# Kernel tuning notes

Measured on AMD Instinct MI355X. Metric: run time of the kernel, lower is better.

The kernel has to match this reference:

```python
import jax, jax.numpy as jnp
import numpy as np

N, E, D, L = 100000, 500000, 128, 5
NUM_ATOM_FEATS, ATOM_VOCAB = 9, 120
NUM_BOND_FEATS, BOND_VOCAB = 3, 8
BN_EPS = 1e-5


def setup_inputs() -> dict:
    key = jax.random.key(0)
    ks = jax.random.split(key, 16)
    inp = {
        "x": jax.random.randint(ks[0], (N, NUM_ATOM_FEATS), 0, ATOM_VOCAB),
        "edge_index": jax.random.randint(ks[1], (2, E), 0, N),
        "edge_attr": jax.random.randint(ks[2], (E, NUM_BOND_FEATS), 0, BOND_VOCAB),
        "edge_weight": jax.random.uniform(ks[3], (E,), dtype=jnp.float32),
        # parameters
        "atom_emb": jax.random.normal(ks[4], (NUM_ATOM_FEATS, ATOM_VOCAB, D), dtype=jnp.float32) * 0.02,
        "bond_emb": jax.random.normal(ks[5], (L, NUM_BOND_FEATS, BOND_VOCAB, D), dtype=jnp.float32) * 0.02,
        "eps": jnp.zeros((L,), dtype=jnp.float32),
        "W1": jax.random.normal(ks[6], (L, D, 2 * D), dtype=jnp.float32) / np.sqrt(D),
        "b1": jnp.zeros((L, 2 * D), dtype=jnp.float32),
        "g1": jnp.ones((L, 2 * D), dtype=jnp.float32),
        "bt1": jnp.zeros((L, 2 * D), dtype=jnp.float32),
        "W2": jax.random.normal(ks[7], (L, 2 * D, D), dtype=jnp.float32) / np.sqrt(2 * D),
        "b2": jnp.zeros((L, D), dtype=jnp.float32),
        "g_out": jnp.ones((L, D), dtype=jnp.float32),
        "bt_out": jnp.zeros((L, D), dtype=jnp.float32),
    }
    return inp


def _batchnorm(h, g, b):
    # training-mode BN over node axis, biased variance (matches torch BN normalization)
    mu = jnp.mean(h, axis=0)
    var = jnp.mean((h - mu) ** 2, axis=0)
    return g * (h - mu) * jax.lax.rsqrt(var + BN_EPS) + b


def reference(x, edge_index, edge_attr, edge_weight,
              atom_emb, bond_emb, eps, W1, b1, g1, bt1, W2, b2, g_out, bt_out):
    # AtomEncoder: sum per-column embedding lookups -> [N, D]
    h = atom_emb[jnp.arange(NUM_ATOM_FEATS)[None, :], x].sum(axis=1)
    src, dst = edge_index[0], edge_index[1]
    ew = edge_weight[:, None]
    for l in range(L):
        # BondEncoder for layer l -> [E, D]
        e = bond_emb[l][jnp.arange(NUM_BOND_FEATS)[None, :], edge_attr].sum(axis=1)
        # message: relu(x_j + edge_emb) * edge_weight ; aggregate: scatter-add at dst
        m = jax.nn.relu(h[src] + e) * ew
        agg = jax.ops.segment_sum(m, dst, num_segments=N)
        z = (1.0 + eps[l]) * h + agg
        # GIN MLP: Linear -> BN -> ReLU -> Linear
        z = jax.nn.relu(_batchnorm(z @ W1[l] + b1[l], g1[l], bt1[l])) @ W2[l] + b2[l]
        # outer BatchNorm; dropout is identity in eval mode
        h_new = _batchnorm(z, g_out[l], bt_out[l])
        h = h_new if l == L - 1 else jax.nn.relu(h_new)
    return h
```

## Files before the change

### kernel.cpp

```cpp
#include <hip/hip_runtime.h>
#include <hip/hip_bf16.h>
#include <hip/hip_fp16.h>

#define NN 100000
#define EE 500000
#define NP 100096

typedef _Float16 f16;
typedef __attribute__((ext_vector_type(8))) _Float16 f16x8;
typedef __attribute__((ext_vector_type(4))) _Float16 f16x4;
typedef __attribute__((ext_vector_type(4))) float f32x4;

static __device__ __forceinline__ f16x8 relu8(f16x8 a) {
#if __has_builtin(__builtin_elementwise_max)
  f16x8 z = {0, 0, 0, 0, 0, 0, 0, 0};
  return __builtin_elementwise_max(a, z);
#else
  f16x8 r;
#pragma unroll
  for (int i = 0; i < 8; ++i) r[i] = (a[i] > (f16)0) ? a[i] : (f16)0;
  return r;
#endif
}

__global__ __launch_bounds__(256) void init_kernel(const float* __restrict__ W1,
                                                   const float* __restrict__ W2,
                                                   f16* __restrict__ w1f,
                                                   f16* __restrict__ w2f,
                                                   int* __restrict__ deg,
                                                   float* __restrict__ slices) {
  int gid = blockIdx.x * 256 + threadIdx.x;
  if (gid < 163840) {
    int l = gid / 32768; int rem = gid % 32768;
    int k = rem / 256;   int n = rem % 256;
    int ctg = n >> 4, m = n & 15;
    int c = k >> 5, q = (k >> 3) & 3, e = k & 7;
    int lane = q * 16 + m;
    w1f[l * 32768 + ((ctg * 4 + c) * 64 + lane) * 8 + e] = (f16)W1[gid];
  } else if (gid < 327680) {
    int g = gid - 163840;
    int l = g / 32768; int rem = g % 32768;
    int k = rem / 128; int n = rem % 128;
    int ctg = n >> 4, m = n & 15;
    int c = k >> 5, q = (k >> 3) & 3, e = k & 7;
    int lane = q * 16 + m;
    w2f[l * 32768 + ((ctg * 8 + c) * 64 + lane) * 8 + e] = (f16)W2[g];
  } else if (gid < 427680) {
    int i = gid - 327680;
    if (i < NN) deg[i] = 0;
  } else if (gid < 439968) {
    slices[gid - 427680] = 0.f;
  }
}

__global__ __launch_bounds__(256) void bondtab_kernel(const float* __restrict__ bemb,
                                                      f16* __restrict__ tab) {
  int gid = blockIdx.x * 256 + threadIdx.x;
  int l = gid >> 16;
  int rem = gid & 65535;
  int combo = rem >> 7, d = rem & 127;
  int a0 = combo & 7, a1 = (combo >> 3) & 7, a2 = combo >> 6;
  const float* bl = bemb + l * 3072;
  float v = bl[a0 * 128 + d] + bl[1024 + a1 * 128 + d] + bl[2048 + a2 * 128 + d];
  tab[gid] = (f16)v;
}

__global__ __launch_bounds__(256) void hist_kernel(const int* __restrict__ ei, int* __restrict__ deg) {
  int e = blockIdx.x * 256 + threadIdx.x;
  if (e < EE) atomicAdd(&deg[ei[EE + e]], 1);
}

__global__ __launch_bounds__(256) void scan1_kernel(const int* __restrict__ deg,
                                                    int* __restrict__ offs,
                                                    int* __restrict__ bsum) {
  __shared__ int sh[256];
  int b = blockIdx.x, t = threadIdx.x;
  int base = b * 1024 + t * 4;
  int v[4];
  int s = 0;
#pragma unroll
  for (int i = 0; i < 4; ++i) { v[i] = (base + i < NN) ? deg[base + i] : 0; s += v[i]; }
  sh[t] = s;
  __syncthreads();
  for (int off = 1; off < 256; off <<= 1) {
    int x = (t >= off) ? sh[t - off] : 0;
    __syncthreads();
    sh[t] += x;
    __syncthreads();
  }
  int excl = sh[t] - s;
  if (t == 255) bsum[b] = sh[255];
  int run = excl;
#pragma unroll
  for (int i = 0; i < 4; ++i) {
    if (base + i < NN) offs[base + i] = run;
    run += v[i];
  }
}

__global__ void scan2_kernel(int* __restrict__ bsum, int nb) {
  if (threadIdx.x == 0 && blockIdx.x == 0) {
    int run = 0;
    for (int i = 0; i < nb; ++i) { int v = bsum[i]; bsum[i] = run; run += v; }
  }
}

__global__ __launch_bounds__(256) void scan3_kernel(int* __restrict__ offs,
                                                    const int* __restrict__ bsum,
                                                    int* __restrict__ cursor) {
  int i = blockIdx.x * 256 + threadIdx.x;
  if (i < NN) {
    int v = offs[i] + bsum[i >> 10];
    offs[i] = v;
    cursor[i] = v;
  } else if (i == NN) {
    offs[NN] = EE;
  }
}

__global__ __launch_bounds__(256) void scatter_kernel(const int* __restrict__ ei,
                                                      const int* __restrict__ ea,
                                                      const float* __restrict__ ew,
                                                      int* __restrict__ cursor,
                                                      int2* __restrict__ pkw) {
  int e = blockIdx.x * 256 + threadIdx.x;
  if (e >= EE) return;
  int dst = ei[EE + e];
  int pos = atomicAdd(&cursor[dst], 1);
  int src = ei[e];
  int a0 = ea[e * 3 + 0], a1 = ea[e * 3 + 1], a2 = ea[e * 3 + 2];
  pkw[pos] = make_int2(src | (a0 << 17) | (a1 << 20) | (a2 << 23), __float_as_int(ew[e]));
}

__global__ __launch_bounds__(256) void atom_kernel(const int* __restrict__ x,
                                                   const float* __restrict__ aemb,
                                                   f16* __restrict__ hf) {
  int gid = blockIdx.x * 256 + threadIdx.x;
  int n = gid >> 5, qq = gid & 31;
  if (n >= NN) return;
  float4 s = {0.f, 0.f, 0.f, 0.f};
#pragma unroll
  for (int f = 0; f < 9; ++f) {
    int xi = x[n * 9 + f];
    float4 v = *(const float4*)(aemb + (f * 120 + xi) * 128 + qq * 4);
    s.x += v.x; s.y += v.y; s.z += v.z; s.w += v.w;
  }
  f16x4 o;
  o[0] = (f16)s.x; o[1] = (f16)s.y; o[2] = (f16)s.z; o[3] = (f16)s.w;
  *(f16x4*)(hf + (long)n * 128 + qq * 4) = o;
}

__global__ __launch_bounds__(256) void edge_agg_kernel(const int* __restrict__ offs,
                                                       const int2* __restrict__ pkw,
                                                       const f16* __restrict__ tab,
                                                       const float* __restrict__ eps,
                                                       const f16* __restrict__ hf,
                                                       f16* __restrict__ zb) {
  int gid = blockIdx.x * 256 + threadIdx.x;
  int n = gid >> 4, d0 = (gid & 15) * 8;
  if (n >= NN) {
    f16x8 z = {0, 0, 0, 0, 0, 0, 0, 0};
    *(f16x8*)(zb + (long)n * 128 + d0) = z;
    return;
  }
  int s0 = offs[n], s1 = offs[n + 1];
  float e1 = 1.f + eps[0];
  f16x8 hn = *(const f16x8*)(hf + (long)n * 128 + d0);
  float acc[8];
#pragma unroll
  for (int i = 0; i < 8; ++i) acc[i] = e1 * (float)hn[i];

  float wA, wB; f16x8 hA, bA, hB, bB;
  if (s0 < s1) {
    int2 pw = pkw[s0]; wA = __int_as_float(pw.y);
    hA = *(const f16x8*)(hf + (long)(pw.x & 131071) * 128 + d0);
    bA = *(const f16x8*)(tab + ((pw.x >> 17) & 511) * 128 + d0);
  }
  if (s0 + 1 < s1) {
    int2 pw = pkw[s0 + 1]; wB = __int_as_float(pw.y);
    hB = *(const f16x8*)(hf + (long)(pw.x & 131071) * 128 + d0);
    bB = *(const f16x8*)(tab + ((pw.x >> 17) & 511) * 128 + d0);
  }
  int e = s0;
  for (; e + 1 < s1; e += 2) {
    {
      f16x8 sm = relu8(hA + bA);
#pragma unroll
      for (int i = 0; i < 8; ++i) acc[i] += (float)sm[i] * wA;
      if (e + 2 < s1) {
        int2 pw = pkw[e + 2]; wA = __int_as_float(pw.y);
        hA = *(const f16x8*)(hf + (long)(pw.x & 131071) * 128 + d0);
        bA = *(const f16x8*)(tab + ((pw.x >> 17) & 511) * 128 + d0);
      }
    }
    {
      f16x8 sm = relu8(hB + bB);
#pragma unroll
      for (int i = 0; i < 8; ++i) acc[i] += (float)sm[i] * wB;
      if (e + 3 < s1) {
        int2 pw = pkw[e + 3]; wB = __int_as_float(pw.y);
        hB = *(const f16x8*)(hf + (long)(pw.x & 131071) * 128 + d0);
        bB = *(const f16x8*)(tab + ((pw.x >> 17) & 511) * 128 + d0);
      }
    }
  }
  if (e < s1) {
    f16x8 sm = relu8(hA + bA);
#pragma unroll
    for (int i = 0; i < 8; ++i) acc[i] += (float)sm[i] * wA;
  }
  f16x8 o;
#pragma unroll
  for (int i = 0; i < 8; ++i) o[i] = (f16)acc[i];
  *(f16x8*)(zb + (long)n * 128 + d0) = o;
}

__global__ __launch_bounds__(256) void edge_agg_bn_kernel(const int* __restrict__ offs,
                                                          const int2* __restrict__ pkw,
                                                          const f16* __restrict__ tab,
                                                          const float* __restrict__ eps, int l,
                                                          const f16* __restrict__ t2,
                                                          const float* __restrict__ sum2s,
                                                          const float* __restrict__ sq2s,
                                                          const float* __restrict__ g2,
                                                          const float* __restrict__ bt2,
                                                          float* __restrict__ s1z,
                                                          f16* __restrict__ zb) {
  __shared__ float sc2[128], sh2[128];
  const int tid = threadIdx.x;
  if (tid < 128) {
    float s = 0.f, s2 = 0.f;
#pragma unroll
    for (int k = 0; k < 16; ++k) { s += sum2s[k * 128 + tid]; s2 += sq2s[k * 128 + tid]; }
    float mu = s * (1.f / NN);
    float var = fmaxf(s2 * (1.f / NN) - mu * mu, 0.f);
    float is = rsqrtf(var + 1e-5f);
    float sc = g2[tid] * is;
    sc2[tid] = sc;
    sh2[tid] = bt2[tid] - mu * sc;
  }
  if (blockIdx.x == 0) {
#pragma unroll
    for (int j = 0; j < 8; ++j)
      *(float4*)(s1z + (j * 256 + tid) * 4) = float4{0.f, 0.f, 0.f, 0.f};
  }
  __syncthreads();
  int gid = blockIdx.x * 256 + tid;
  int n = gid >> 4, d0 = (gid & 15) * 8;
  if (n >= NN) {
    f16x8 z = {0, 0, 0, 0, 0, 0, 0, 0};
    *(f16x8*)(zb + (long)n * 128 + d0) = z;
    return;
  }
  float4 svA = *(const float4*)(sc2 + d0), svB = *(const float4*)(sc2 + d0 + 4);
  float4 shA = *(const float4*)(sh2 + d0), shB = *(const float4*)(sh2 + d0 + 4);
  float sv[8] = {svA.x, svA.y, svA.z, svA.w, svB.x, svB.y, svB.z, svB.w};
  float hv[8] = {shA.x, shA.y, shA.z, shA.w, shB.x, shB.y, shB.z, shB.w};
  f16x8 sv8, hv8;
#pragma unroll
  for (int i = 0; i < 8; ++i) { sv8[i] = (f16)sv[i]; hv8[i] = (f16)hv[i]; }

  int s0 = offs[n], s1 = offs[n + 1];
  float e1 = 1.f + eps[l];
  f16x8 hn = *(const f16x8*)(t2 + (long)n * 128 + d0);
  float acc[8];
#pragma unroll
  for (int i = 0; i < 8; ++i)
    acc[i] = e1 * fmaxf((float)hn[i] * sv[i] + hv[i], 0.f);

  float wA, wB; f16x8 hA, bA, hB, bB;
  if (s0 < s1) {
    int2 pw = pkw[s0]; wA = __int_as_float(pw.y);
    hA = *(const f16x8*)(t2 + (long)(pw.x & 131071) * 128 + d0);
    bA = *(const f16x8*)(tab + ((pw.x >> 17) & 511) * 128 + d0);
  }
  if (s0 + 1 < s1) {
    int2 pw = pkw[s0 + 1]; wB = __int_as_float(pw.y);
    hB = *(const f16x8*)(t2 + (long)(pw.x & 131071) * 128 + d0);
    bB = *(const f16x8*)(tab + ((pw.x >> 17) & 511) * 128 + d0);
  }
  int e = s0;
  for (; e + 1 < s1; e += 2) {
    {
      f16x8 y = relu8(hA * sv8 + hv8);
      f16x8 sm = relu8(y + bA);
#pragma unroll
      for (int i = 0; i < 8; ++i) acc[i] += (float)sm[i] * wA;
      if (e + 2 < s1) {
        int2 pw = pkw[e + 2]; wA = __int_as_float(pw.y);
        hA = *(const f16x8*)(t2 + (long)(pw.x & 131071) * 128 + d0);
        bA = *(const f16x8*)(tab + ((pw.x >> 17) & 511) * 128 + d0);
      }
    }
    {
      f16x8 y = relu8(hB * sv8 + hv8);
      f16x8 sm = relu8(y + bB);
#pragma unroll
      for (int i = 0; i < 8; ++i) acc[i] += (float)sm[i] * wB;
      if (e + 3 < s1) {
        int2 pw = pkw[e + 3]; wB = __int_as_float(pw.y);
        hB = *(const f16x8*)(t2 + (long)(pw.x & 131071) * 128 + d0);
        bB = *(const f16x8*)(tab + ((pw.x >> 17) & 511) * 128 + d0);
      }
    }
  }
  if (e < s1) {
    f16x8 y = relu8(hA * sv8 + hv8);
    f16x8 sm = relu8(y + bA);
#pragma unroll
    for (int i = 0; i < 8; ++i) acc[i] += (float)sm[i] * wA;
  }
  f16x8 o;
#pragma unroll
  for (int i = 0; i < 8; ++i) o[i] = (f16)acc[i];
  *(f16x8*)(zb + (long)n * 128 + d0) = o;
}

__global__ __launch_bounds__(256) void gemm1_kernel(const f16* __restrict__ zb,
                                                    const f16* __restrict__ w1f,
                                                    f16* __restrict__ t1f,
                                                    float* __restrict__ sum1s,
                                                    float* __restrict__ sq1s,
                                                    float* __restrict__ s2z) {
  __shared__ __align__(16) char ldsraw[17408];
  const int tid = threadIdx.x;
  const int lane = tid & 63, w = tid >> 6;
  const int wr = w >> 1, wc = w & 1;
  const int m = lane & 15, q = lane >> 4;
  const int rbase = blockIdx.x * 64;
  const int slice = blockIdx.x & 15;

  if (blockIdx.x == 0) {
#pragma unroll
    for (int j = 0; j < 4; ++j)
      *(float4*)(s2z + (j * 256 + tid) * 4) = float4{0.f, 0.f, 0.f, 0.f};
  }

  {
    f16x8 st[4];
    const int tofs = tid * 16;
#pragma unroll
    for (int j = 0; j < 4; ++j)
      st[j] = *(const f16x8*)(zb + (long)rbase * 128 + (tofs + j * 4096) / 2);
#pragma unroll
    for (int j = 0; j < 4; ++j) {
      int ofs = tofs + j * 4096;
      int row = ofs >> 8, colb = ofs & 255;
      *(f16x8*)(ldsraw + row * 256 + (colb ^ ((row & 7) << 4))) = st[j];
    }
  }
  __syncthreads();

  f16x8 A[2][4];
#pragma unroll
  for (int rt = 0; rt < 2; ++rt) {
    int row = wr * 32 + rt * 16 + m;
    int rs = row * 256, sw = (row & 7) << 4;
#pragma unroll
    for (int c = 0; c < 4; ++c) {
      int colb = c * 64 + q * 16;
      A[rt][c] = *(const f16x8*)(ldsraw + rs + (colb ^ sw));
    }
  }
  __syncthreads();

  f16 (*sh)[136] = (f16(*)[136])ldsraw;
  const int colc = tid & 15, r0 = tid >> 4;

#pragma unroll
  for (int h = 0; h < 2; ++h) {
    f16x8 B[4][4];
#pragma unroll
    for (int ct = 0; ct < 4; ++ct)
#pragma unroll
      for (int c = 0; c < 4; ++c)
        B[ct][c] = *(const f16x8*)(w1f + (((h * 8 + wc * 4 + ct) * 4 + c) * 64 + lane) * 8);

    f32x4 acc[2][4];
    const f32x4 zf = {0.f, 0.f, 0.f, 0.f};
#pragma unroll
    for (int a = 0; a < 2; ++a)
#pragma unroll
      for (int b = 0; b < 4; ++b) acc[a][b] = zf;
#pragma unroll
    for (int c = 0; c < 4; ++c)
#pragma unroll
      for (int rt = 0; rt < 2; ++rt)
#pragma unroll
        for (int ct = 0; ct < 4; ++ct)
          acc[rt][ct] = __builtin_amdgcn_mfma_f32_16x16x32_f16(A[rt][c], B[ct][c], acc[rt][ct], 0, 0, 0);

#pragma unroll
    for (int ct = 0; ct < 4; ++ct) {
      int lc = wc * 64 + ct * 16 + m;
      int gc = h * 128 + lc;
      float s = 0.f, s2 = 0.f;
#pragma unroll
      for (int rt = 0; rt < 2; ++rt) {
        int lr = wr * 32 + rt * 16 + q * 4;
#pragma unroll
        for (int i = 0; i < 4; ++i) {
          float v = acc[rt][ct][i];
          s += v; s2 += v * v;
          sh[lr + i][lc] = (f16)v;
        }
      }
      s  += __shfl_xor(s, 16);  s  += __shfl_xor(s, 32);
      s2 += __shfl_xor(s2, 16); s2 += __shfl_xor(s2, 32);
      if (q == 0) {
        unsafeAtomicAdd(&sum1s[slice * 256 + gc], s);
        unsafeAtomicAdd(&sq1s[slice * 256 + gc], s2);
      }
    }
    __syncthreads();
#pragma unroll
    for (int j = 0; j < 4; ++j) {
      int r = j * 16 + r0;
      f16x8 v = *(const f16x8*)(&sh[r][colc * 8]);
      *(f16x8*)(t1f + (long)(rbase + r) * 256 + h * 128 + colc * 8) = v;
    }
    __syncthreads();
  }
}

__global__ __launch_bounds__(256) void gemm2_kernel(const f16* __restrict__ a1,
                                                    const f16* __restrict__ w2f,
                                                    const float* __restrict__ sum1s,
                                                    const float* __restrict__ sq1s,
                                                    const float* __restrict__ g1,
                                                    const float* __restrict__ bt1,
                                                    f16* __restrict__ t2out,
                                                    float* __restrict__ sum2s,
                                                    float* __restrict__ sq2s) {
  __shared__ __align__(16) char ldsraw[34816];
  float* sc1 = (float*)(ldsraw + 32768);
  float* sh1 = (float*)(ldsraw + 33792);
  const int tid = threadIdx.x;
  const int lane = tid & 63, w = tid >> 6;
  const int wr = w >> 1, wc = w & 1;
  const int m = lane & 15, q = lane >> 4;
  const int rbase = blockIdx.x * 64;
  const int slice = blockIdx.x & 15;

  f16x8 st[8];
  const int tofs = tid * 16;
#pragma unroll
  for (int j = 0; j < 8; ++j)
    st[j] = *(const f16x8*)(a1 + (long)rbase * 256 + (tofs + j * 4096) / 2);

  {
    float s = 0.f, s2 = 0.f;
#pragma unroll
    for (int k = 0; k < 16; ++k) { s += sum1s[k * 256 + tid]; s2 += sq1s[k * 256 + tid]; }
    float mu = s * (1.f / NN);
    float var = fmaxf(s2 * (1.f / NN) - mu * mu, 0.f);
    float is = rsqrtf(var + 1e-5f);
    float sc = g1[tid] * is;
    sc1[tid] = sc;
    sh1[tid] = bt1[tid] - mu * sc;
  }
  __syncthreads();

  {
    const int k0 = (tid & 31) * 8;
    float4 sa = *(const float4*)(sc1 + k0);
    float4 sb = *(const float4*)(sc1 + k0 + 4);
    float4 ha = *(const float4*)(sh1 + k0);
    float4 hb = *(const float4*)(sh1 + k0 + 4);
#pragma unroll
    for (int j = 0; j < 8; ++j) {
      int ofs = tofs + j * 4096;
      int row = ofs >> 9, colb = ofs & 511;
      f16x8 u = st[j], o;
      o[0] = (f16)fmaxf((float)u[0] * sa.x + ha.x, 0.f);
      o[1] = (f16)fmaxf((float)u[1] * sa.y + ha.y, 0.f);
      o[2] = (f16)fmaxf((float)u[2] * sa.z + ha.z, 0.f);
      o[3] = (f16)fmaxf((float)u[3] * sa.w + ha.w, 0.f);
      o[4] = (f16)fmaxf((float)u[4] * sb.x + hb.x, 0.f);
      o[5] = (f16)fmaxf((float)u[5] * sb.y + hb.y, 0.f);
      o[6] = (f16)fmaxf((float)u[6] * sb.z + hb.z, 0.f);
      o[7] = (f16)fmaxf((float)u[7] * sb.w + hb.w, 0.f);
      *(f16x8*)(ldsraw + row * 512 + (colb ^ ((row & 7) << 4))) = o;
    }
  }
  __syncthreads();

  f32x4 acc[2][4];
  const f32x4 zf = {0.f, 0.f, 0.f, 0.f};
#pragma unroll
  for (int a = 0; a < 2; ++a)
#pragma unroll
    for (int b = 0; b < 4; ++b) acc[a][b] = zf;

#pragma unroll
  for (int hh = 0; hh < 2; ++hh) {
    f16x8 A[2][4], B[4][4];
#pragma unroll
    for (int rt = 0; rt < 2; ++rt) {
      int row = wr * 32 + rt * 16 + m;
      int rs = row * 512, sw = (row & 7) << 4;
#pragma unroll
      for (int c = 0; c < 4; ++c) {
        int colb = (hh * 4 + c) * 64 + q * 16;
        A[rt][c] = *(const f16x8*)(ldsraw + rs + (colb ^ sw));
      }
    }
#pragma unroll
    for (int ct = 0; ct < 4; ++ct)
#pragma unroll
      for (int c = 0; c < 4; ++c)
        B[ct][c] = *(const f16x8*)(w2f + (((wc * 4 + ct) * 8 + hh * 4 + c) * 64 + lane) * 8);
#pragma unroll
    for (int c = 0; c < 4; ++c)
#pragma unroll
      for (int rt = 0; rt < 2; ++rt)
#pragma unroll
        for (int ct = 0; ct < 4; ++ct)
          acc[rt][ct] = __builtin_amdgcn_mfma_f32_16x16x32_f16(A[rt][c], B[ct][c], acc[rt][ct], 0, 0, 0);
  }

  __syncthreads();
  f16 (*sh)[136] = (f16(*)[136])ldsraw;

#pragma unroll
  for (int ct = 0; ct < 4; ++ct) {
    int gc = wc * 64 + ct * 16 + m;
    float s = 0.f, s2 = 0.f;
#pragma unroll
    for (int rt = 0; rt < 2; ++rt) {
      int grow = rbase + wr * 32 + rt * 16 + q * 4;
      int lr = wr * 32 + rt * 16 + q * 4;
#pragma unroll
      for (int i = 0; i < 4; ++i) {
        float v = acc[rt][ct][i];
        float vv = (grow + i < NN) ? v : 0.f;
        s += vv; s2 += vv * vv;
        sh[lr + i][gc] = (f16)v;
      }
    }
    s  += __shfl_xor(s, 16);  s  += __shfl_xor(s, 32);
    s2 += __shfl_xor(s2, 16); s2 += __shfl_xor(s2, 32);
    if (q == 0) {
      unsafeAtomicAdd(&sum2s[slice * 128 + gc], s);
      unsafeAtomicAdd(&sq2s[slice * 128 + gc], s2);
    }
  }
  __syncthreads();
  const int colc = tid & 15, r0 = tid >> 4;
#pragma unroll
  for (int j = 0; j < 4; ++j) {
    int r = j * 16 + r0;
    f16x8 v = *(const f16x8*)(&sh[r][colc * 8]);
    *(f16x8*)(t2out + (long)(rbase + r) * 128 + colc * 8) = v;
  }
}

__global__ __launch_bounds__(256) void apply_kernel(const f16* __restrict__ t2,
                                                    const float* __restrict__ sum2s,
                                                    const float* __restrict__ sq2s,
                                                    const float* __restrict__ g2,
                                                    const float* __restrict__ bt2,
                                                    float* __restrict__ outp) {
  __shared__ float sc2[128], sh2[128];
  const int tid = threadIdx.x;
  if (tid < 128) {
    float s = 0.f, s2 = 0.f;
#pragma unroll
    for (int k = 0; k < 16; ++k) { s += sum2s[k * 128 + tid]; s2 += sq2s[k * 128 + tid]; }
    float mu = s * (1.f / NN);
    float var = fmaxf(s2 * (1.f / NN) - mu * mu, 0.f);
    float is = rsqrtf(var + 1e-5f);
    float sc = g2[tid] * is;
    sc2[tid] = sc;
    sh2[tid] = bt2[tid] - mu * sc;
  }
  __syncthreads();
  const int rbase = blockIdx.x * 64;
#pragma unroll
  for (int k = 0; k < 4; ++k) {
    int ci = tid + k * 256;
    int r = ci >> 4, c8 = ci & 15;
    int row = rbase + r;
    if (row >= NN) continue;
    f16x8 u = *(const f16x8*)(t2 + (long)row * 128 + c8 * 8);
    float4 sa = *(const float4*)(sc2 + c8 * 8);
    float4 sb = *(const float4*)(sc2 + c8 * 8 + 4);
    float4 ha = *(const float4*)(sh2 + c8 * 8);
    float4 hb = *(const float4*)(sh2 + c8 * 8 + 4);
    float4 o0 = {(float)u[0] * sa.x + ha.x, (float)u[1] * sa.y + ha.y,
                 (float)u[2] * sa.z + ha.z, (float)u[3] * sa.w + ha.w};
    float4 o1 = {(float)u[4] * sb.x + hb.x, (float)u[5] * sb.y + hb.y,
                 (float)u[6] * sb.z + hb.z, (float)u[7] * sb.w + hb.w};
    *(float4*)(outp + (long)row * 128 + c8 * 8) = o0;
    *(float4*)(outp + (long)row * 128 + c8 * 8 + 4) = o1;
  }
}

extern "C" void kernel_launch(void* const* d_in, const int* in_sizes, int n_in,
                              void* d_out, int out_size, void* d_ws, size_t ws_size,
                              hipStream_t stream) {
  (void)in_sizes; (void)n_in; (void)out_size; (void)ws_size;
  const int*   x      = (const int*)d_in[0];
  const int*   ei     = (const int*)d_in[1];
  const int*   ea     = (const int*)d_in[2];
  const float* ew     = (const float*)d_in[3];
  const float* aemb   = (const float*)d_in[4];
  const float* bemb   = (const float*)d_in[5];
  const float* eps    = (const float*)d_in[6];
  const float* W1     = (const float*)d_in[7];
  const float* g1     = (const float*)d_in[9];
  const float* bt1    = (const float*)d_in[10];
  const float* W2     = (const float*)d_in[11];
  const float* g_out  = (const float*)d_in[13];
  const float* bt_out = (const float*)d_in[14];

  float* outp = (float*)d_out;

  char* ws = (char*)d_ws;
  f16*   hf    = (f16*)(ws);
  f16*   zb    = (f16*)(ws + 25624576);
  f16*   t1f   = (f16*)(ws + 51249152);
  f16*   w1f   = (f16*)(ws + 102498304);
  f16*   w2f   = (f16*)(ws + 102825984);
  float* slices= (float*)(ws + 103153664);
  int*   offs  = (int*)(ws + 103202816);
  int*   bsum  = (int*)(ws + 103602848);
  int*   deg   = (int*)(ws + 103603360);
  int*   cursor= (int*)(ws + 104003360);
  f16*   bsumtab = (f16*)(ws + 103603360);
  int2*  pkw   = (int2*)(ws + 104403360);

  float* sum1s = slices;
  float* sq1s  = slices + 4096;
  float* sum2s = slices + 8192;
  float* sq2s  = slices + 10240;

  init_kernel<<<1719, 256, 0, stream>>>(W1, W2, w1f, w2f, deg, slices);
  hist_kernel<<<1954, 256, 0, stream>>>(ei, deg);
  scan1_kernel<<<98, 256, 0, stream>>>(deg, offs, bsum);
  scan2_kernel<<<1, 64, 0, stream>>>(bsum, 98);
  scan3_kernel<<<392, 256, 0, stream>>>(offs, bsum, cursor);
  scatter_kernel<<<1954, 256, 0, stream>>>(ei, ea, ew, cursor, pkw);
  bondtab_kernel<<<1280, 256, 0, stream>>>(bemb, bsumtab);
  atom_kernel<<<12500, 256, 0, stream>>>(x, aemb, hf);

  for (int l = 0; l < 5; ++l) {
    if (l == 0) {
      edge_agg_kernel<<<6256, 256, 0, stream>>>(offs, pkw, bsumtab, eps, hf, zb);
    } else {
      edge_agg_bn_kernel<<<6256, 256, 0, stream>>>(offs, pkw, bsumtab + l * 65536, eps, l,
                                                   hf, sum2s, sq2s,
                                                   g_out + (l - 1) * 128, bt_out + (l - 1) * 128,
                                                   sum1s, zb);
    }
    gemm1_kernel<<<1564, 256, 0, stream>>>(zb, w1f + l * 32768, t1f, sum1s, sq1s, sum2s);
    gemm2_kernel<<<1564, 256, 0, stream>>>(t1f, w2f + l * 32768, sum1s, sq1s,
                                           g1 + l * 256, bt1 + l * 256, hf, sum2s, sq2s);
    if (l == 4)
      apply_kernel<<<1564, 256, 0, stream>>>(hf, sum2s, sq2s, g_out + 512, bt_out + 512, outp);
  }
}
```

Before: 597.1 us.

## Sort nodes by degree for edge aggregation and split gemm1 over column halves

Adds a counting sort of nodes by in-degree (histogram, scan, scatter kernels) and makes the edge aggregation kernels process nodes in that order, so neighbouring threads handle nodes with similar edge counts and wavefront divergence drops. Separately, gemm1 now launches a 2D grid where each block computes one 128-column half of the 256-wide output instead of looping over both halves. This doubles parallelism and cuts per-block register use for B, but the A tile is loaded twice. The sort adds three small preprocessing launches and scatters zb writes in node order, giving less write locality.

```diff
diff --git a/kernel.cpp b/kernel.cpp
--- a/kernel.cpp
+++ b/kernel.cpp
@@ -28,7 +28,8 @@
                                                    f16* __restrict__ w1f,
                                                    f16* __restrict__ w2f,
                                                    int* __restrict__ deg,
-                                                   float* __restrict__ slices) {
+                                                   float* __restrict__ slices,
+                                                   int* __restrict__ dmeta) {
   int gid = blockIdx.x * 256 + threadIdx.x;
   if (gid < 163840) {
     int l = gid / 32768; int rem = gid % 32768;
@@ -50,6 +51,8 @@
     if (i < NN) deg[i] = 0;
   } else if (gid < 439968) {
     slices[gid - 427680] = 0.f;
+  } else if (gid < 440096) {
+    dmeta[gid - 439968] = 0;
   }
 }
 
@@ -132,6 +135,48 @@
   pkw[pos] = make_int2(src | (a0 << 17) | (a1 << 20) | (a2 << 23), __float_as_int(ew[e]));
 }
 
+__global__ __launch_bounds__(256) void dhist_kernel(const int* __restrict__ deg,
+                                                    int* __restrict__ dhist) {
+  __shared__ int lh[64];
+  int t = threadIdx.x;
+  if (t < 64) lh[t] = 0;
+  __syncthreads();
+  int n = blockIdx.x * 256 + t;
+  if (n < NN) {
+    int d = deg[n]; if (d > 63) d = 63;
+    atomicAdd(&lh[d], 1);
+  }
+  __syncthreads();
+  if (t < 64 && lh[t] > 0) atomicAdd(&dhist[t], lh[t]);
+}
+
+__global__ void dscan_kernel(const int* __restrict__ dhist, int* __restrict__ dcur) {
+  if (threadIdx.x == 0 && blockIdx.x == 0) {
+    int run = 0;
+    for (int i = 0; i < 64; ++i) { int v = dhist[i]; dcur[i] = run; run += v; }
+  }
+}
+
+__global__ __launch_bounds__(256) void dscatter_kernel(const int* __restrict__ deg,
+                                                       int* __restrict__ dcur,
+                                                       int* __restrict__ norder) {
+  __shared__ int lcnt[64], lbase[64];
+  int t = threadIdx.x;
+  if (t < 64) lcnt[t] = 0;
+  __syncthreads();
+  int n = blockIdx.x * 256 + t;
+  int b = 0, lpos = 0;
+  bool valid = (n < NN);
+  if (valid) {
+    b = deg[n]; if (b > 63) b = 63;
+    lpos = atomicAdd(&lcnt[b], 1);
+  }
+  __syncthreads();
+  if (t < 64 && lcnt[t] > 0) lbase[t] = atomicAdd(&dcur[t], lcnt[t]);
+  __syncthreads();
+  if (valid) norder[lbase[b] + lpos] = n;
+}
+
 __global__ __launch_bounds__(256) void atom_kernel(const int* __restrict__ x,
                                                    const float* __restrict__ aemb,
                                                    f16* __restrict__ hf) {
@@ -154,15 +199,17 @@
                                                        const int2* __restrict__ pkw,
                                                        const f16* __restrict__ tab,
                                                        const float* __restrict__ eps,
+                                                       const int* __restrict__ norder,
                                                        const f16* __restrict__ hf,
                                                        f16* __restrict__ zb) {
   int gid = blockIdx.x * 256 + threadIdx.x;
-  int n = gid >> 4, d0 = (gid & 15) * 8;
-  if (n >= NN) {
+  int g = gid >> 4, d0 = (gid & 15) * 8;
+  if (g >= NN) {
     f16x8 z = {0, 0, 0, 0, 0, 0, 0, 0};
-    *(f16x8*)(zb + (long)n * 128 + d0) = z;
+    *(f16x8*)(zb + (long)g * 128 + d0) = z;
     return;
   }
+  int n = norder[g];
   int s0 = offs[n], s1 = offs[n + 1];
   float e1 = 1.f + eps[0];
   f16x8 hn = *(const f16x8*)(hf + (long)n * 128 + d0);
@@ -219,6 +266,7 @@
                                                           const int2* __restrict__ pkw,
                                                           const f16* __restrict__ tab,
                                                           const float* __restrict__ eps, int l,
+                                                          const int* __restrict__ norder,
                                                           const f16* __restrict__ t2,
                                                           const float* __restrict__ sum2s,
                                                           const float* __restrict__ sq2s,
@@ -246,12 +294,13 @@
   }
   __syncthreads();
   int gid = blockIdx.x * 256 + tid;
-  int n = gid >> 4, d0 = (gid & 15) * 8;
-  if (n >= NN) {
+  int g = gid >> 4, d0 = (gid & 15) * 8;
+  if (g >= NN) {
     f16x8 z = {0, 0, 0, 0, 0, 0, 0, 0};
-    *(f16x8*)(zb + (long)n * 128 + d0) = z;
+    *(f16x8*)(zb + (long)g * 128 + d0) = z;
     return;
   }
+  int n = norder[g];
   float4 svA = *(const float4*)(sc2 + d0), svB = *(const float4*)(sc2 + d0 + 4);
   float4 shA = *(const float4*)(sh2 + d0), shB = *(const float4*)(sh2 + d0 + 4);
   float sv[8] = {svA.x, svA.y, svA.z, svA.w, svB.x, svB.y, svB.z, svB.w};
@@ -327,14 +376,22 @@
   const int lane = tid & 63, w = tid >> 6;
   const int wr = w >> 1, wc = w & 1;
   const int m = lane & 15, q = lane >> 4;
-  const int rbase = blockIdx.x * 64;
-  const int slice = blockIdx.x & 15;
-
-  if (blockIdx.x == 0) {
+  const int cb = blockIdx.x;
+  const int rbase = blockIdx.y * 64;
+  const int slice = blockIdx.y & 15;
+
+  if (blockIdx.y == 0 && cb == 0) {
 #pragma unroll
     for (int j = 0; j < 4; ++j)
       *(float4*)(s2z + (j * 256 + tid) * 4) = float4{0.f, 0.f, 0.f, 0.f};
   }
+
+  f16x8 B[4][4];
+#pragma unroll
+  for (int ct = 0; ct < 4; ++ct)
+#pragma unroll
+    for (int c = 0; c < 4; ++c)
+      B[ct][c] = *(const f16x8*)(w1f + (((cb * 8 + wc * 4 + ct) * 4 + c) * 64 + lane) * 8);
 
   {
     f16x8 st[4];
@@ -362,64 +419,54 @@
       A[rt][c] = *(const f16x8*)(ldsraw + rs + (colb ^ sw));
     }
   }
-  __syncthreads();
-
+
+  f32x4 acc[2][4];
+  const f32x4 zf = {0.f, 0.f, 0.f, 0.f};
+#pragma unroll
+  for (int a = 0; a < 2; ++a)
+#pragma unroll
+    for (int b = 0; b < 4; ++b) acc[a][b] = zf;
+
+#pragma unroll
+  for (int c = 0; c < 4; ++c)
+#pragma unroll
+    for (int rt = 0; rt < 2; ++rt)
+#pragma unroll
+      for (int ct = 0; ct < 4; ++ct)
+        acc[rt][ct] = __builtin_amdgcn_mfma_f32_16x16x32_f16(A[rt][c], B[ct][c], acc[rt][ct], 0, 0, 0);
+
+  __syncthreads();
   f16 (*sh)[136] = (f16(*)[136])ldsraw;
+
+#pragma unroll
+  for (int ct = 0; ct < 4; ++ct) {
+    int lc = wc * 64 + ct * 16 + m;
+    int gc = cb * 128 + lc;
+    float s = 0.f, s2 = 0.f;
+#pragma unroll
+    for (int rt = 0; rt < 2; ++rt) {
+      int lr = wr * 32 + rt * 16 + q * 4;
+#pragma unroll
+      for (int i = 0; i < 4; ++i) {
+        float v = acc[rt][ct][i];
+        s += v; s2 += v * v;
+        sh[lr + i][lc] = (f16)v;
+      }
+    }
+    s  += __shfl_xor(s, 16);  s  += __shfl_xor(s, 32);
+    s2 += __shfl_xor(s2, 16); s2 += __shfl_xor(s2, 32);
+    if (q == 0) {
+      unsafeAtomicAdd(&sum1s[slice * 256 + gc], s);
+      unsafeAtomicAdd(&sq1s[slice * 256 + gc], s2);
+    }
+  }
+  __syncthreads();
   const int colc = tid & 15, r0 = tid >> 4;
-
-#pragma unroll
-  for (int h = 0; h < 2; ++h) {
-    f16x8 B[4][4];
-#pragma unroll
-    for (int ct = 0; ct < 4; ++ct)
-#pragma unroll
-      for (int c = 0; c < 4; ++c)
-        B[ct][c] = *(const f16x8*)(w1f + (((h * 8 + wc * 4 + ct) * 4 + c) * 64 + lane) * 8);
-
-    f32x4 acc[2][4];
-    const f32x4 zf = {0.f, 0.f, 0.f, 0.f};
-#pragma unroll
-    for (int a = 0; a < 2; ++a)
-#pragma unroll
-      for (int b = 0; b < 4; ++b) acc[a][b] = zf;
-#pragma unroll
-    for (int c = 0; c < 4; ++c)
-#pragma unroll
-      for (int rt = 0; rt < 2; ++rt)
-#pragma unroll
-        for (int ct = 0; ct < 4; ++ct)
-          acc[rt][ct] = __builtin_amdgcn_mfma_f32_16x16x32_f16(A[rt][c], B[ct][c], acc[rt][ct], 0, 0, 0);
-
-#pragma unroll
-    for (int ct = 0; ct < 4; ++ct) {
-      int lc = wc * 64 + ct * 16 + m;
-      int gc = h * 128 + lc;
-      float s = 0.f, s2 = 0.f;
-#pragma unroll
-      for (int rt = 0; rt < 2; ++rt) {
-        int lr = wr * 32 + rt * 16 + q * 4;
-#pragma unroll
-        for (int i = 0; i < 4; ++i) {
-          float v = acc[rt][ct][i];
-          s += v; s2 += v * v;
-          sh[lr + i][lc] = (f16)v;
-        }
-      }
-      s  += __shfl_xor(s, 16);  s  += __shfl_xor(s, 32);
-      s2 += __shfl_xor(s2, 16); s2 += __shfl_xor(s2, 32);
-      if (q == 0) {
-        unsafeAtomicAdd(&sum1s[slice * 256 + gc], s);
-        unsafeAtomicAdd(&sq1s[slice * 256 + gc], s2);
-      }
-    }
-    __syncthreads();
-#pragma unroll
-    for (int j = 0; j < 4; ++j) {
-      int r = j * 16 + r0;
-      f16x8 v = *(const f16x8*)(&sh[r][colc * 8]);
-      *(f16x8*)(t1f + (long)(rbase + r) * 256 + h * 128 + colc * 8) = v;
-    }
-    __syncthreads();
+#pragma unroll
+  for (int j = 0; j < 4; ++j) {
+    int r = j * 16 + r0;
+    f16x8 v = *(const f16x8*)(&sh[r][colc * 8]);
+    *(f16x8*)(t1f + (long)(rbase + r) * 256 + cb * 128 + colc * 8) = v;
   }
 }
 
@@ -629,31 +676,39 @@
   int*   cursor= (int*)(ws + 104003360);
   f16*   bsumtab = (f16*)(ws + 103603360);
   int2*  pkw   = (int2*)(ws + 104403360);
+  int*   norder= (int*)(ws + 108403360);
+  int*   dmeta = (int*)(ws + 108803744);
+
+  int* dhist = dmeta;
+  int* dcur  = dmeta + 64;
 
   float* sum1s = slices;
   float* sq1s  = slices + 4096;
   float* sum2s = slices + 8192;
   float* sq2s  = slices + 10240;
 
-  init_kernel<<<1719, 256, 0, stream>>>(W1, W2, w1f, w2f, deg, slices);
+  init_kernel<<<1720, 256, 0, stream>>>(W1, W2, w1f, w2f, deg, slices, dmeta);
   hist_kernel<<<1954, 256, 0, stream>>>(ei, deg);
   scan1_kernel<<<98, 256, 0, stream>>>(deg, offs, bsum);
   scan2_kernel<<<1, 64, 0, stream>>>(bsum, 98);
   scan3_kernel<<<392, 256, 0, stream>>>(offs, bsum, cursor);
   scatter_kernel<<<1954, 256, 0, stream>>>(ei, ea, ew, cursor, pkw);
+  dhist_kernel<<<391, 256, 0, stream>>>(deg, dhist);
+  dscan_kernel<<<1, 64, 0, stream>>>(dhist, dcur);
+  dscatter_kernel<<<391, 256, 0, stream>>>(deg, dcur, norder);
   bondtab_kernel<<<1280, 256, 0, stream>>>(bemb, bsumtab);
   atom_kernel<<<12500, 256, 0, stream>>>(x, aemb, hf);
 
   for (int l = 0; l < 5; ++l) {
     if (l == 0) {
-      edge_agg_kernel<<<6256, 256, 0, stream>>>(offs, pkw, bsumtab, eps, hf, zb);
+      edge_agg_kernel<<<6256, 256, 0, stream>>>(offs, pkw, bsumtab, eps, norder, hf, zb);
     } else {
       edge_agg_bn_kernel<<<6256, 256, 0, stream>>>(offs, pkw, bsumtab + l * 65536, eps, l,
-                                                   hf, sum2s, sq2s,
+                                                   norder, hf, sum2s, sq2s,
                                                    g_out + (l - 1) * 128, bt_out + (l - 1) * 128,
                                                    sum1s, zb);
     }
-    gemm1_kernel<<<1564, 256, 0, stream>>>(zb, w1f + l * 32768, t1f, sum1s, sq1s, sum2s);
+    gemm1_kernel<<<dim3(2, 1564), 256, 0, stream>>>(zb, w1f + l * 32768, t1f, sum1s, sq1s, sum2s);
     gemm2_kernel<<<1564, 256, 0, stream>>>(t1f, w2f + l * 32768, sum1s, sq1s,
                                            g1 + l * 256, bt1 + l * 256, hf, sum2s, sq2s);
     if (l == 4)
```

Measured after the change: 588.9 us, median of 2. Within noise of the previous version (-1.4%).
